# Performance work log

Hardware: AMD Instinct MI355X
Metric: run time of the kernel (lower is better)

## Reference

```python
import jax, jax.numpy as jnp
import numpy as np

N, S, R, CM = 1, 128, 256, 256
C, CZ = 32, 128


def setup_inputs() -> dict:
    key = jax.random.key(0)
    k1, k2, k3, k4 = jax.random.split(key, 4)
    return {
        "msa_repr": jax.random.normal(k1, (N, S, R, CM), dtype=jnp.float32),
        "left_proj": jax.random.normal(k2, (CM, C), dtype=jnp.float32) * 0.05,
        "right_proj": jax.random.normal(k3, (CM, C), dtype=jnp.float32) * 0.05,
        "out_proj": jax.random.normal(k4, (C * C, CZ), dtype=jnp.float32) * 0.05,
    }


def reference(msa_repr, left_proj, right_proj, out_proj):
    # msa_repr: [N, S, R, CM]
    # Project to left/right activations and move R before S
    # (equivalent to torch matmul + transpose(-2, -3)).
    a = jnp.einsum("nsrm,mc->nrsc", msa_repr, left_proj)   # [N, R, S, C]
    b = jnp.einsum("nsrm,mc->nrsc", msa_repr, right_proj)  # [N, R, S, C]
    # Outer product contracted over the MSA dim S:
    # outer[n, r, t, c, e] = sum_s a[n, r, s, c] * b[n, t, s, e]
    outer = jnp.einsum("nrsc,ntse->nrtce", a, b)            # [N, R, R, C, C]
    n, r, t = outer.shape[:3]
    outer = outer.reshape(n, r, t, C * C)                   # [N, R, R, C*C]
    # Output projection to pair channels cz
    return outer @ out_proj                                 # [N, R, R, CZ]
```

## Files before the change

### kernel.cpp

```cpp
#include <hip/hip_runtime.h>

typedef __bf16 bf16x8 __attribute__((ext_vector_type(8)));
typedef __bf16 bf16x4 __attribute__((ext_vector_type(4)));
typedef float f32x16 __attribute__((ext_vector_type(16)));
typedef float f32x4 __attribute__((ext_vector_type(4)));

constexpr int S = 128, R = 256, CM = 256, C = 32, CZ = 128;

#define MFMA __builtin_amdgcn_mfma_f32_32x32x16_bf16

__device__ __forceinline__ bf16x4 cvt4(float a, float b, float c, float d) {
    bf16x4 r;
    r[0] = (__bf16)a; r[1] = (__bf16)b; r[2] = (__bf16)c; r[3] = (__bf16)d;
    return r;
}

__global__ __launch_bounds__(256) void k_wt(const float* __restrict__ W,
                                            __bf16* __restrict__ WTf) {
    int g = blockIdx.x * 256 + threadIdx.x;
    int cz = g & 127;
    int k = g >> 7;
    int e = k >> 5, c = k & 31;
    float v = W[(size_t)(c * 32 + e) * 128 + cz];
    WTf[((size_t)(k >> 3) * 128 + cz) * 8 + (k & 7)] = (__bf16)v;
}

__global__ __launch_bounds__(256) void k_wlr(const float* __restrict__ Lp,
                                             const float* __restrict__ Rp,
                                             __bf16* __restrict__ WLRT) {
    int c = blockIdx.x;
    int m = threadIdx.x;
    const float* src = (c < 32) ? Lp : Rp;
    WLRT[(size_t)c * 256 + m] = (__bf16)src[(size_t)m * 32 + (c & 31)];
}

__global__ __launch_bounds__(256) void k_proj(const float* __restrict__ msa,
                                              const __bf16* __restrict__ WLRT,
                                              __bf16* __restrict__ aTf,
                                              __bf16* __restrict__ bTf) {
    __shared__ __align__(16) __bf16 As[64 * 256];
    const int r = blockIdx.x;
    const int sh = blockIdx.y;
    const int t = threadIdx.x;

#pragma unroll 4
    for (int it = 0; it < 16; ++it) {
        int idx = it * 256 + t;
        int row = idx >> 6;
        int cg = idx & 63;
        float4 v = *(const float4*)&msa[((size_t)(sh * 64 + row) * R + r) * CM + cg * 4];
        bf16x4 h = cvt4(v.x, v.y, v.z, v.w);
        int P = (cg >> 1) ^ (row & 15);
        *(bf16x4*)((char*)As + row * 512 + P * 16 + (cg & 1) * 8) = h;
    }
    __syncthreads();

    const int w = t >> 6;
    const int l31 = t & 31;
    const int kh = (t >> 5) & 1;
    const int sd = w & 1;
    const int mi = w >> 1;

    f32x16 acc;
#pragma unroll
    for (int q = 0; q < 16; ++q) acc[q] = 0.f;

    const bf16x8* wb = (const bf16x8*)&WLRT[(size_t)(sd * 32 + l31) * 256 + 8 * kh];
    const int srow = mi * 32 + l31;
    const char* arow = (const char*)As + srow * 512;

    __builtin_amdgcn_s_setprio(1);
#pragma unroll
    for (int ks = 0; ks < 16; ++ks) {
        int P = (2 * ks + kh) ^ (srow & 15);
        bf16x8 af = *(const bf16x8*)(arow + P * 16);
        acc = MFMA(af, wb[2 * ks], acc, 0, 0, 0);
    }
    __builtin_amdgcn_s_setprio(0);

    __bf16* dst = sd ? bTf : aTf;
    const int wg = sh * 2 + mi;
#pragma unroll
    for (int q = 0; q < 4; ++q) {
        size_t base = (size_t)r * 4096 + (size_t)(2 * wg + (q >> 1)) * 512 +
                      (size_t)(q & 1) * 256 + (size_t)l31 * 8 + 4 * kh;
        *(bf16x4*)&dst[base] = cvt4(acc[4 * q + 0], acc[4 * q + 1],
                                    acc[4 * q + 2], acc[4 * q + 3]);
    }
}

__global__ __launch_bounds__(512, 2) void k_main(const __bf16* __restrict__ aTf,
                                                 const __bf16* __restrict__ bTf,
                                                 const __bf16* __restrict__ WTf,
                                                 float* __restrict__ out) {
    __shared__ __align__(16) __bf16 Gs[64 * 1024];

    const int t = threadIdx.x;
    const int w = t >> 6;
    const int l = t & 63;
    const int lane = l & 31;
    const int kh = l >> 5;
    const int r0 = blockIdx.x * 8;
    const int t0 = blockIdx.y * 8;

    const int rg = w >> 1;
    const int tg = w & 1;

    f32x16 acc[2][4];
#pragma unroll
    for (int i = 0; i < 2; ++i)
#pragma unroll
        for (int j = 0; j < 4; ++j)
#pragma unroll
            for (int q = 0; q < 16; ++q) acc[i][j][q] = 0.f;

    const bf16x8* ap0 = (const bf16x8*)aTf + ((size_t)(r0 + 2 * rg + 0) * 512 + kh * 32 + lane);
    const bf16x8* ap1 = (const bf16x8*)aTf + ((size_t)(r0 + 2 * rg + 1) * 512 + kh * 32 + lane);
    const bf16x8* bp0 = (const bf16x8*)bTf + ((size_t)(t0 + 4 * tg + 0) * 512 + kh * 32 + lane);
    const bf16x8* bp1 = (const bf16x8*)bTf + ((size_t)(t0 + 4 * tg + 1) * 512 + kh * 32 + lane);
    const bf16x8* bp2 = (const bf16x8*)bTf + ((size_t)(t0 + 4 * tg + 2) * 512 + kh * 32 + lane);
    const bf16x8* bp3 = (const bf16x8*)bTf + ((size_t)(t0 + 4 * tg + 3) * 512 + kh * 32 + lane);

    bf16x8 A0[2], B0[4], A1[2], B1[4];
#define LDA(Aa, Bb, ks) do { \
    Aa[0] = ap0[(ks) * 64]; Aa[1] = ap1[(ks) * 64]; \
    Bb[0] = bp0[(ks) * 64]; Bb[1] = bp1[(ks) * 64]; \
    Bb[2] = bp2[(ks) * 64]; Bb[3] = bp3[(ks) * 64]; } while (0)
#define PH_A(Aa, Bb) do { \
    __builtin_amdgcn_s_setprio(1); \
    acc[0][0] = MFMA(Aa[0], Bb[0], acc[0][0], 0, 0, 0); \
    acc[0][1] = MFMA(Aa[0], Bb[1], acc[0][1], 0, 0, 0); \
    acc[0][2] = MFMA(Aa[0], Bb[2], acc[0][2], 0, 0, 0); \
    acc[0][3] = MFMA(Aa[0], Bb[3], acc[0][3], 0, 0, 0); \
    acc[1][0] = MFMA(Aa[1], Bb[0], acc[1][0], 0, 0, 0); \
    acc[1][1] = MFMA(Aa[1], Bb[1], acc[1][1], 0, 0, 0); \
    acc[1][2] = MFMA(Aa[1], Bb[2], acc[1][2], 0, 0, 0); \
    acc[1][3] = MFMA(Aa[1], Bb[3], acc[1][3], 0, 0, 0); \
    __builtin_amdgcn_s_setprio(0); } while (0)

    LDA(A0, B0, 0);
#pragma unroll
    for (int ks = 0; ks < 8; ks += 2) {
        LDA(A1, B1, ks + 1);
        PH_A(A0, B0);
        LDA(A0, B0, (ks + 2) & 7);
        PH_A(A1, B1);
    }

#pragma unroll
    for (int i = 0; i < 2; ++i) {
#pragma unroll
        for (int j = 0; j < 4; ++j) {
            int p = (2 * rg + i) * 8 + 4 * tg + j;
            unsigned prow = (unsigned)p * 2048;
#pragma unroll
            for (int q = 0; q < 4; ++q) {
                int Lc = lane * 4 + q;
                int P = Lc ^ (p & 15) ^ (lane & 7);
                *(bf16x4*)((char*)Gs + prow + (unsigned)P * 16 + kh * 8) =
                    cvt4(acc[i][j][4 * q + 0], acc[i][j][4 * q + 1],
                         acc[i][j][4 * q + 2], acc[i][j][4 * q + 3]);
            }
        }
    }
    __syncthreads();

    const int kq = w >> 1;
    const int ng = w & 1;
    const int czl0 = ng * 64 + lane;
    const int czl1 = czl0 + 32;
    const bf16x8* wb0 = (const bf16x8*)WTf + ((size_t)kh * 128 + czl0);
    const bf16x8* wb1 = (const bf16x8*)WTf + ((size_t)kh * 128 + czl1);
    const unsigned prow0 = (unsigned)lane * 2048;
    const unsigned prow1 = (unsigned)(lane + 32) * 2048;
    const int p15 = lane & 15;

    f32x16 o00, o01, o10, o11;
#pragma unroll
    for (int q = 0; q < 16; ++q) { o00[q] = 0.f; o01[q] = 0.f; o10[q] = 0.f; o11[q] = 0.f; }

    bf16x8 Wa0, Wa1, Ga0, Ga1, Wb0_, Wb1_, Gb0, Gb1;
#define LDB(W0v, W1v, G0v, G1v, kk) do { \
    W0v = wb0[(size_t)(kk) * 256]; \
    W1v = wb1[(size_t)(kk) * 256]; \
    int Lr = (kk) * 2 + kh; \
    int P = Lr ^ p15 ^ ((Lr >> 2) & 7); \
    G0v = *(const bf16x8*)((const char*)Gs + prow0 + (unsigned)P * 16); \
    G1v = *(const bf16x8*)((const char*)Gs + prow1 + (unsigned)P * 16); } while (0)
#define PHB(W0v, W1v, G0v, G1v) do { \
    __builtin_amdgcn_s_setprio(1); \
    o00 = MFMA(G0v, W0v, o00, 0, 0, 0); \
    o01 = MFMA(G0v, W1v, o01, 0, 0, 0); \
    o10 = MFMA(G1v, W0v, o10, 0, 0, 0); \
    o11 = MFMA(G1v, W1v, o11, 0, 0, 0); \
    __builtin_amdgcn_s_setprio(0); } while (0)

    LDB(Wa0, Wa1, Ga0, Ga1, kq * 16);
#pragma unroll
    for (int j = 0; j < 16; j += 2) {
        LDB(Wb0_, Wb1_, Gb0, Gb1, kq * 16 + ((j + 1) & 15));
        PHB(Wa0, Wa1, Ga0, Ga1);
        LDB(Wa0, Wa1, Ga0, Ga1, kq * 16 + ((j + 2) & 15));
        PHB(Wb0_, Wb1_, Gb0, Gb1);
    }
    __syncthreads();

    {
        char* pr = (char*)Gs + (size_t)w * 16384;
        const f32x16* os[4] = {&o00, &o01, &o10, &o11};
#pragma unroll
        for (int s2 = 0; s2 < 4; ++s2) {
#pragma unroll
            for (int pc = 0; pc < 4; ++pc) {
                f32x4 v;
                v[0] = (*os[s2])[4 * pc + 0]; v[1] = (*os[s2])[4 * pc + 1];
                v[2] = (*os[s2])[4 * pc + 2]; v[3] = (*os[s2])[4 * pc + 3];
                *(f32x4*)(pr + ((s2 * 4 + pc) * 64 + l) * 16) = v;
            }
        }
    }
    __syncthreads();

    {
        const int ngx = w >> 2;
        const int mix = (w >> 1) & 1;
        const int nix = w & 1;
        const int s2 = mix * 2 + nix;
        f32x16 sm;
#pragma unroll
        for (int q = 0; q < 16; ++q) sm[q] = 0.f;
#pragma unroll
        for (int kq2 = 0; kq2 < 4; ++kq2) {
            const char* pr = (const char*)Gs + (size_t)(kq2 * 2 + ngx) * 16384;
#pragma unroll
            for (int pc = 0; pc < 4; ++pc) {
                f32x4 v = *(const f32x4*)(pr + ((s2 * 4 + pc) * 64 + l) * 16);
                sm[4 * pc + 0] += v[0]; sm[4 * pc + 1] += v[1];
                sm[4 * pc + 2] += v[2]; sm[4 * pc + 3] += v[3];
            }
        }
        const int czl = ngx * 64 + nix * 32 + (l & 31);
        const int khx = l >> 5;
#pragma unroll
        for (int reg = 0; reg < 16; ++reg) {
            int pl = mix * 32 + (reg & 3) + 8 * (reg >> 2) + 4 * khx;
            int prr = pl >> 3, ptt = pl & 7;
            out[((size_t)(r0 + prr) * 256 + (t0 + ptt)) * 128 + czl] = sm[reg];
        }
    }
}

extern "C" void kernel_launch(void* const* d_in, const int* in_sizes, int n_in,
                              void* d_out, int out_size, void* d_ws, size_t ws_size,
                              hipStream_t stream) {
    const float* msa = (const float*)d_in[0];
    const float* left = (const float*)d_in[1];
    const float* right = (const float*)d_in[2];
    const float* W = (const float*)d_in[3];

    __bf16* aTf = (__bf16*)d_ws;
    __bf16* bTf = aTf + (size_t)R * 4096;
    __bf16* WTf = bTf + (size_t)R * 4096;
    __bf16* WLRT = WTf + (size_t)128 * 1024;
    float* outp = (float*)d_out;

    k_wt<<<512, 256, 0, stream>>>(W, WTf);
    k_wlr<<<64, 256, 0, stream>>>(left, right, WLRT);
    k_proj<<<dim3(256, 2), 256, 0, stream>>>(msa, WLRT, aTf, bTf);
    k_main<<<dim3(32, 32), 512, 0, stream>>>(aTf, bTf, WTf, outp);
}
```

Before: 60.61 us.

## Merge prep kernels, split projection K across waves, deepen main-loop prefetch

Fuses the two weight-conversion kernels into one launch to save a kernel launch. The projection kernel now uses 4 S-quarters per row with a split-K across wave pairs, reduced through shared memory, which doubles block count and halves LDS per block. k_main swaps the wave-to-tile mapping and replaces the double-buffered loads with a 3-stage (first GEMM) and 5-stage (second GEMM) register prefetch ring. The deeper prefetch raises register pressure under the 512x2 launch bounds and could cause spills.

```diff
diff --git a/kernel.cpp b/kernel.cpp
--- a/kernel.cpp
+++ b/kernel.cpp
@@ -15,40 +15,43 @@
     return r;
 }
 
-__global__ __launch_bounds__(256) void k_wt(const float* __restrict__ W,
-                                            __bf16* __restrict__ WTf) {
-    int g = blockIdx.x * 256 + threadIdx.x;
-    int cz = g & 127;
-    int k = g >> 7;
-    int e = k >> 5, c = k & 31;
-    float v = W[(size_t)(c * 32 + e) * 128 + cz];
-    WTf[((size_t)(k >> 3) * 128 + cz) * 8 + (k & 7)] = (__bf16)v;
-}
-
-__global__ __launch_bounds__(256) void k_wlr(const float* __restrict__ Lp,
-                                             const float* __restrict__ Rp,
-                                             __bf16* __restrict__ WLRT) {
-    int c = blockIdx.x;
-    int m = threadIdx.x;
-    const float* src = (c < 32) ? Lp : Rp;
-    WLRT[(size_t)c * 256 + m] = (__bf16)src[(size_t)m * 32 + (c & 31)];
+__global__ __launch_bounds__(256) void k_prep(const float* __restrict__ W,
+                                              const float* __restrict__ Lp,
+                                              const float* __restrict__ Rp,
+                                              __bf16* __restrict__ WTf,
+                                              __bf16* __restrict__ WLRT) {
+    int b = blockIdx.x;
+    if (b < 512) {
+        int g = b * 256 + threadIdx.x;
+        int cz = g & 127;
+        int k = g >> 7;
+        int e = k >> 5, c = k & 31;
+        float v = W[(size_t)(c * 32 + e) * 128 + cz];
+        WTf[((size_t)(k >> 3) * 128 + cz) * 8 + (k & 7)] = (__bf16)v;
+    } else {
+        int c = b - 512;
+        int m = threadIdx.x;
+        const float* src = (c < 32) ? Lp : Rp;
+        WLRT[(size_t)c * 256 + m] = (__bf16)src[(size_t)m * 32 + (c & 31)];
+    }
 }
 
 __global__ __launch_bounds__(256) void k_proj(const float* __restrict__ msa,
                                               const __bf16* __restrict__ WLRT,
                                               __bf16* __restrict__ aTf,
                                               __bf16* __restrict__ bTf) {
-    __shared__ __align__(16) __bf16 As[64 * 256];
+    __shared__ __align__(16) __bf16 As[32 * 256];
+    __shared__ __align__(16) char Pp[2 * 4096];
     const int r = blockIdx.x;
-    const int sh = blockIdx.y;
+    const int sq = blockIdx.y;
     const int t = threadIdx.x;
 
-#pragma unroll 4
-    for (int it = 0; it < 16; ++it) {
+#pragma unroll
+    for (int it = 0; it < 8; ++it) {
         int idx = it * 256 + t;
         int row = idx >> 6;
         int cg = idx & 63;
-        float4 v = *(const float4*)&msa[((size_t)(sh * 64 + row) * R + r) * CM + cg * 4];
+        float4 v = *(const float4*)&msa[((size_t)(sq * 32 + row) * R + r) * CM + cg * 4];
         bf16x4 h = cvt4(v.x, v.y, v.z, v.w);
         int P = (cg >> 1) ^ (row & 15);
         *(bf16x4*)((char*)As + row * 512 + P * 16 + (cg & 1) * 8) = h;
@@ -56,36 +59,55 @@
     __syncthreads();
 
     const int w = t >> 6;
+    const int l = t & 63;
     const int l31 = t & 31;
     const int kh = (t >> 5) & 1;
     const int sd = w & 1;
-    const int mi = w >> 1;
+    const int ksh = w >> 1;
 
     f32x16 acc;
 #pragma unroll
     for (int q = 0; q < 16; ++q) acc[q] = 0.f;
 
     const bf16x8* wb = (const bf16x8*)&WLRT[(size_t)(sd * 32 + l31) * 256 + 8 * kh];
-    const int srow = mi * 32 + l31;
-    const char* arow = (const char*)As + srow * 512;
+    const char* arow = (const char*)As + l31 * 512;
 
     __builtin_amdgcn_s_setprio(1);
 #pragma unroll
-    for (int ks = 0; ks < 16; ++ks) {
-        int P = (2 * ks + kh) ^ (srow & 15);
+    for (int j = 0; j < 8; ++j) {
+        int ks = ksh * 8 + j;
+        int P = (2 * ks + kh) ^ (l31 & 15);
         bf16x8 af = *(const bf16x8*)(arow + P * 16);
         acc = MFMA(af, wb[2 * ks], acc, 0, 0, 0);
     }
     __builtin_amdgcn_s_setprio(0);
 
-    __bf16* dst = sd ? bTf : aTf;
-    const int wg = sh * 2 + mi;
-#pragma unroll
-    for (int q = 0; q < 4; ++q) {
-        size_t base = (size_t)r * 4096 + (size_t)(2 * wg + (q >> 1)) * 512 +
-                      (size_t)(q & 1) * 256 + (size_t)l31 * 8 + 4 * kh;
-        *(bf16x4*)&dst[base] = cvt4(acc[4 * q + 0], acc[4 * q + 1],
-                                    acc[4 * q + 2], acc[4 * q + 3]);
+    char* pbase = Pp + (size_t)sd * 4096;
+    if (ksh == 1) {
+#pragma unroll
+        for (int pc = 0; pc < 4; ++pc) {
+            f32x4 v;
+            v[0] = acc[4 * pc + 0]; v[1] = acc[4 * pc + 1];
+            v[2] = acc[4 * pc + 2]; v[3] = acc[4 * pc + 3];
+            *(f32x4*)(pbase + ((pc * 64) + l) * 16) = v;
+        }
+    }
+    __syncthreads();
+    if (ksh == 0) {
+#pragma unroll
+        for (int pc = 0; pc < 4; ++pc) {
+            f32x4 v = *(const f32x4*)(pbase + ((pc * 64) + l) * 16);
+            acc[4 * pc + 0] += v[0]; acc[4 * pc + 1] += v[1];
+            acc[4 * pc + 2] += v[2]; acc[4 * pc + 3] += v[3];
+        }
+        __bf16* dst = sd ? bTf : aTf;
+#pragma unroll
+        for (int q = 0; q < 4; ++q) {
+            size_t base = (size_t)r * 4096 + (size_t)(2 * sq + (q >> 1)) * 512 +
+                          (size_t)(q & 1) * 256 + (size_t)l31 * 8 + 4 * kh;
+            *(bf16x4*)&dst[base] = cvt4(acc[4 * q + 0], acc[4 * q + 1],
+                                        acc[4 * q + 2], acc[4 * q + 3]);
+        }
     }
 }
 
@@ -103,8 +125,8 @@
     const int r0 = blockIdx.x * 8;
     const int t0 = blockIdx.y * 8;
 
-    const int rg = w >> 1;
-    const int tg = w & 1;
+    const int rg = w & 3;
+    const int tg = w >> 2;
 
     f32x16 acc[2][4];
 #pragma unroll
@@ -121,30 +143,32 @@
     const bf16x8* bp2 = (const bf16x8*)bTf + ((size_t)(t0 + 4 * tg + 2) * 512 + kh * 32 + lane);
     const bf16x8* bp3 = (const bf16x8*)bTf + ((size_t)(t0 + 4 * tg + 3) * 512 + kh * 32 + lane);
 
-    bf16x8 A0[2], B0[4], A1[2], B1[4];
-#define LDA(Aa, Bb, ks) do { \
-    Aa[0] = ap0[(ks) * 64]; Aa[1] = ap1[(ks) * 64]; \
-    Bb[0] = bp0[(ks) * 64]; Bb[1] = bp1[(ks) * 64]; \
-    Bb[2] = bp2[(ks) * 64]; Bb[3] = bp3[(ks) * 64]; } while (0)
-#define PH_A(Aa, Bb) do { \
-    __builtin_amdgcn_s_setprio(1); \
-    acc[0][0] = MFMA(Aa[0], Bb[0], acc[0][0], 0, 0, 0); \
-    acc[0][1] = MFMA(Aa[0], Bb[1], acc[0][1], 0, 0, 0); \
-    acc[0][2] = MFMA(Aa[0], Bb[2], acc[0][2], 0, 0, 0); \
-    acc[0][3] = MFMA(Aa[0], Bb[3], acc[0][3], 0, 0, 0); \
-    acc[1][0] = MFMA(Aa[1], Bb[0], acc[1][0], 0, 0, 0); \
-    acc[1][1] = MFMA(Aa[1], Bb[1], acc[1][1], 0, 0, 0); \
-    acc[1][2] = MFMA(Aa[1], Bb[2], acc[1][2], 0, 0, 0); \
-    acc[1][3] = MFMA(Aa[1], Bb[3], acc[1][3], 0, 0, 0); \
-    __builtin_amdgcn_s_setprio(0); } while (0)
-
-    LDA(A0, B0, 0);
-#pragma unroll
-    for (int ks = 0; ks < 8; ks += 2) {
-        LDA(A1, B1, ks + 1);
-        PH_A(A0, B0);
-        LDA(A0, B0, (ks + 2) & 7);
-        PH_A(A1, B1);
+    bf16x8 Ap[3][2], Bp[3][4];
+#pragma unroll
+    for (int s = 0; s < 3; ++s) {
+        Ap[s][0] = ap0[s * 64]; Ap[s][1] = ap1[s * 64];
+        Bp[s][0] = bp0[s * 64]; Bp[s][1] = bp1[s * 64];
+        Bp[s][2] = bp2[s * 64]; Bp[s][3] = bp3[s * 64];
+    }
+#pragma unroll
+    for (int ks = 0; ks < 8; ++ks) {
+        const int s = ks % 3;
+        __builtin_amdgcn_s_setprio(1);
+        acc[0][0] = MFMA(Ap[s][0], Bp[s][0], acc[0][0], 0, 0, 0);
+        acc[0][1] = MFMA(Ap[s][0], Bp[s][1], acc[0][1], 0, 0, 0);
+        acc[0][2] = MFMA(Ap[s][0], Bp[s][2], acc[0][2], 0, 0, 0);
+        acc[0][3] = MFMA(Ap[s][0], Bp[s][3], acc[0][3], 0, 0, 0);
+        acc[1][0] = MFMA(Ap[s][1], Bp[s][0], acc[1][0], 0, 0, 0);
+        acc[1][1] = MFMA(Ap[s][1], Bp[s][1], acc[1][1], 0, 0, 0);
+        acc[1][2] = MFMA(Ap[s][1], Bp[s][2], acc[1][2], 0, 0, 0);
+        acc[1][3] = MFMA(Ap[s][1], Bp[s][3], acc[1][3], 0, 0, 0);
+        __builtin_amdgcn_s_setprio(0);
+        if (ks + 3 < 8) {
+            const int kn = ks + 3;
+            Ap[s][0] = ap0[kn * 64]; Ap[s][1] = ap1[kn * 64];
+            Bp[s][0] = bp0[kn * 64]; Bp[s][1] = bp1[kn * 64];
+            Bp[s][2] = bp2[kn * 64]; Bp[s][3] = bp3[kn * 64];
+        }
     }
 
 #pragma unroll
@@ -179,29 +203,35 @@
 #pragma unroll
     for (int q = 0; q < 16; ++q) { o00[q] = 0.f; o01[q] = 0.f; o10[q] = 0.f; o11[q] = 0.f; }
 
-    bf16x8 Wa0, Wa1, Ga0, Ga1, Wb0_, Wb1_, Gb0, Gb1;
-#define LDB(W0v, W1v, G0v, G1v, kk) do { \
-    W0v = wb0[(size_t)(kk) * 256]; \
-    W1v = wb1[(size_t)(kk) * 256]; \
-    int Lr = (kk) * 2 + kh; \
-    int P = Lr ^ p15 ^ ((Lr >> 2) & 7); \
-    G0v = *(const bf16x8*)((const char*)Gs + prow0 + (unsigned)P * 16); \
-    G1v = *(const bf16x8*)((const char*)Gs + prow1 + (unsigned)P * 16); } while (0)
-#define PHB(W0v, W1v, G0v, G1v) do { \
-    __builtin_amdgcn_s_setprio(1); \
-    o00 = MFMA(G0v, W0v, o00, 0, 0, 0); \
-    o01 = MFMA(G0v, W1v, o01, 0, 0, 0); \
-    o10 = MFMA(G1v, W0v, o10, 0, 0, 0); \
-    o11 = MFMA(G1v, W1v, o11, 0, 0, 0); \
-    __builtin_amdgcn_s_setprio(0); } while (0)
-
-    LDB(Wa0, Wa1, Ga0, Ga1, kq * 16);
-#pragma unroll
-    for (int j = 0; j < 16; j += 2) {
-        LDB(Wb0_, Wb1_, Gb0, Gb1, kq * 16 + ((j + 1) & 15));
-        PHB(Wa0, Wa1, Ga0, Ga1);
-        LDB(Wa0, Wa1, Ga0, Ga1, kq * 16 + ((j + 2) & 15));
-        PHB(Wb0_, Wb1_, Gb0, Gb1);
+    bf16x8 Wp[5][2], Gp[5][2];
+#pragma unroll
+    for (int s = 0; s < 5; ++s) {
+        const int kk = kq * 16 + s;
+        Wp[s][0] = wb0[(size_t)kk * 256];
+        Wp[s][1] = wb1[(size_t)kk * 256];
+        int Lr = kk * 2 + kh;
+        int P = Lr ^ p15 ^ ((Lr >> 2) & 7);
+        Gp[s][0] = *(const bf16x8*)((const char*)Gs + prow0 + (unsigned)P * 16);
+        Gp[s][1] = *(const bf16x8*)((const char*)Gs + prow1 + (unsigned)P * 16);
+    }
+#pragma unroll
+    for (int j = 0; j < 16; ++j) {
+        const int s = j % 5;
+        __builtin_amdgcn_s_setprio(1);
+        o00 = MFMA(Gp[s][0], Wp[s][0], o00, 0, 0, 0);
+        o01 = MFMA(Gp[s][0], Wp[s][1], o01, 0, 0, 0);
+        o10 = MFMA(Gp[s][1], Wp[s][0], o10, 0, 0, 0);
+        o11 = MFMA(Gp[s][1], Wp[s][1], o11, 0, 0, 0);
+        __builtin_amdgcn_s_setprio(0);
+        if (j + 5 < 16) {
+            const int kk = kq * 16 + j + 5;
+            Wp[s][0] = wb0[(size_t)kk * 256];
+            Wp[s][1] = wb1[(size_t)kk * 256];
+            int Lr = kk * 2 + kh;
+            int P = Lr ^ p15 ^ ((Lr >> 2) & 7);
+            Gp[s][0] = *(const bf16x8*)((const char*)Gs + prow0 + (unsigned)P * 16);
+            Gp[s][1] = *(const bf16x8*)((const char*)Gs + prow1 + (unsigned)P * 16);
+        }
     }
     __syncthreads();
 
@@ -264,8 +294,7 @@
     __bf16* WLRT = WTf + (size_t)128 * 1024;
     float* outp = (float*)d_out;
 
-    k_wt<<<512, 256, 0, stream>>>(W, WTf);
-    k_wlr<<<64, 256, 0, stream>>>(left, right, WLRT);
-    k_proj<<<dim3(256, 2), 256, 0, stream>>>(msa, WLRT, aTf, bTf);
+    k_prep<<<576, 256, 0, stream>>>(W, left, right, WTf, WLRT);
+    k_proj<<<dim3(256, 4), 256, 0, stream>>>(msa, WLRT, aTf, bTf);
     k_main<<<dim3(32, 32), 512, 0, stream>>>(aTf, bTf, WTf, outp);
 }
```

Result: faster. 59.09 us (-2.5%).
